# Performance work log

Hardware: AMD Instinct MI355X
Metric: run time of the kernel (lower is better)

## Reference

```python
import jax, jax.numpy as jnp
import numpy as np
from jax import lax

SEQ_LEN, N_FEAT, N_EMB, N_ENC, BATCH = 100, 18, 16, 16, 16384


def lstm(x, W_ih, W_hh, b_ih, b_hh, hidden):
    """PyTorch-convention LSTM (gates i,f,g,o), batch_first x: [B,T,I].
    Returns (h_seq [B,T,H], h_last [B,H])."""
    B = x.shape[0]
    # Precompute input projections for all timesteps: [B,T,4H]
    xg = jnp.einsum('bti,gi->btg', x, W_ih) + b_ih + b_hh
    W_hh_T = W_hh.T  # [H,4H]

    def step(carry, xg_t):
        h, c = carry
        g = xg_t + h @ W_hh_T                       # [B,4H]
        i, f, gg, o = jnp.split(g, 4, axis=-1)
        i = jax.nn.sigmoid(i)
        f = jax.nn.sigmoid(f)
        gg = jnp.tanh(gg)
        o = jax.nn.sigmoid(o)
        c = f * c + i * gg
        h = o * jnp.tanh(c)
        return (h, c), h

    h0 = jnp.zeros((B, hidden), x.dtype)
    c0 = jnp.zeros((B, hidden), x.dtype)
    (h_last, _), h_seq = lax.scan(step, (h0, c0), jnp.swapaxes(xg, 0, 1))
    return jnp.swapaxes(h_seq, 0, 1), h_last


def setup_inputs() -> dict:
    key = jax.random.key(0)
    ks = jax.random.split(key, 9)
    s1 = 1.0 / np.sqrt(N_EMB)
    s2 = 1.0 / np.sqrt(N_ENC)
    u = lambda k, shape, s: jax.random.uniform(k, shape, jnp.float32, -s, s)
    return {
        'x': jax.random.normal(ks[0], (BATCH, SEQ_LEN, N_FEAT), jnp.float32),
        'W_ih1': u(ks[1], (4 * N_EMB, N_FEAT), s1),
        'W_hh1': u(ks[2], (4 * N_EMB, N_EMB), s1),
        'b_ih1': u(ks[3], (4 * N_EMB,), s1),
        'b_hh1': u(ks[4], (4 * N_EMB,), s1),
        'W_ih2': u(ks[5], (4 * N_ENC, N_EMB), s2),
        'W_hh2': u(ks[6], (4 * N_ENC, N_ENC), s2),
        'b_ih2': u(ks[7], (4 * N_ENC,), s2),
        'b_hh2': u(ks[8], (4 * N_ENC,), s2),
    }


def reference(x, W_ih1, W_hh1, b_ih1, b_hh1, W_ih2, W_hh2, b_ih2, b_hh2):
    h1_seq, _ = lstm(x, W_ih1, W_hh1, b_ih1, b_hh1, N_EMB)
    h1_seq = jax.nn.relu(h1_seq)
    _, h2_last = lstm(h1_seq, W_ih2, W_hh2, b_ih2, b_hh2, N_ENC)
    return jax.nn.relu(h2_last)  # [B, N_ENC]
```

## Files before the change

kernel.cpp:

```cpp
#include <hip/hip_runtime.h>


typedef float f32x4 __attribute__((ext_vector_type(4)));
typedef __bf16 bf16x8 __attribute__((ext_vector_type(8)));
typedef unsigned int uint32x4 __attribute__((ext_vector_type(4)));

union FragU { bf16x8 v; unsigned short u[8]; unsigned int d[4]; uint32x4 q; };

#define MFMA16(A, B, C) __builtin_amdgcn_mfma_f32_16x16x32_bf16((A), (B), (C), 0, 0, 0)

static __device__ __forceinline__ unsigned short f2bf(float f) {
  unsigned int u = __builtin_bit_cast(unsigned int, f);
  u = u + 0x7FFFu + ((u >> 16) & 1u);
  return (unsigned short)(u >> 16);
}
static __device__ __forceinline__ float bfbits2f(unsigned short h) {
  unsigned int u = ((unsigned int)h) << 16;
  return __builtin_bit_cast(float, u);
}
static __device__ __forceinline__ float sigm(float x) {
  return __builtin_amdgcn_rcpf(1.0f + __builtin_amdgcn_exp2f(x * -1.4426950408889634f));
}
static __device__ __forceinline__ float tanh_(float x) {
  return 1.0f - 2.0f * __builtin_amdgcn_rcpf(1.0f + __builtin_amdgcn_exp2f(x * 2.8853900817779268f));
}
static __device__ __forceinline__ unsigned int split_pack(float v) {
  unsigned int u = __builtin_bit_cast(unsigned int, v);
  float hf = __builtin_bit_cast(float, u & 0xFFFF0000u);
  unsigned int l = __builtin_bit_cast(unsigned int, v - hf);
  return (u >> 16) | (l & 0xFFFF0000u);
}
static __device__ __forceinline__ void cvt_pair(float f0, float f1,
                                                unsigned int& hd, unsigned int& ld) {
  unsigned int u0 = __builtin_bit_cast(unsigned int, f0);
  unsigned int u1 = __builtin_bit_cast(unsigned int, f1);
  unsigned int h0 = u0 & 0xFFFF0000u;
  unsigned int h1 = u1 & 0xFFFF0000u;
  hd = (u0 >> 16) | h1;
  unsigned int l0 = __builtin_bit_cast(unsigned int, f0 - __builtin_bit_cast(float, h0));
  unsigned int l1 = __builtin_bit_cast(unsigned int, f1 - __builtin_bit_cast(float, h1));
  ld = (l0 >> 16) | (l1 & 0xFFFF0000u);
}

struct RawX { float2 a, b2, c, d; };

__global__ __launch_bounds__(256, 1) void enc_kernel(
    const float* __restrict__ x,
    const float* __restrict__ Wih1,
    const float* __restrict__ Whh1,
    const float* __restrict__ bih1,
    const float* __restrict__ bhh1,
    const float* __restrict__ Wih2,
    const float* __restrict__ Whh2,
    const float* __restrict__ bih2,
    const float* __restrict__ bhh2,
    float* __restrict__ out)
{
  const int lane = threadIdx.x & 63;
  const int b    = lane & 15;
  const int g    = lane >> 4;

  const int wid = (int)((blockIdx.x * blockDim.x + threadIdx.x) >> 6);
  const int b0  = wid * 16;

  FragU A1h[4], A1l[4], A2h[4], A2l[4], A3h[4], A3l[4], A4h[4], A4l[4];
  f32x4 bias1v[4], bias2v[4];
#pragma unroll
  for (int tn = 0; tn < 4; ++tn) {
    const int row = tn * 16 + b;
#pragma unroll
    for (int j = 0; j < 8; ++j) {
      const int k = 8 * g + j;
      if (k < 18) {
        const float w = Wih1[row * 18 + k];
        A1h[tn].u[j] = f2bf(w);
        A1l[tn].u[j] = f2bf(w - bfbits2f(A1h[tn].u[j]));
      } else {
        A1h[tn].u[j] = 0;
        A1l[tn].u[j] = 0;
      }
      const int kk = k >> 1;
      const float w2 = Whh1[row * 16 + kk];
      const float w3 = Wih2[row * 16 + kk];
      const float w4 = Whh2[row * 16 + kk];
      A2h[tn].u[j] = f2bf(w2); A2l[tn].u[j] = f2bf(w2 - bfbits2f(A2h[tn].u[j]));
      A3h[tn].u[j] = f2bf(w3); A3l[tn].u[j] = f2bf(w3 - bfbits2f(A3h[tn].u[j]));
      A4h[tn].u[j] = f2bf(w4); A4l[tn].u[j] = f2bf(w4 - bfbits2f(A4h[tn].u[j]));
    }
#pragma unroll
    for (int r = 0; r < 4; ++r) {
      const int u4 = tn * 16 + 4 * g + r;
      bias1v[tn][r] = bih1[u4] + bhh1[u4];
      bias2v[tn][r] = bih2[u4] + bhh2[u4];
    }
  }

  const float* const x0 = x + (size_t)(b0 + b) * 1800 + 8 * g;
  const int adv = (g == 3) ? 0 : 18;

  auto loadraw = [&](const float* p) -> RawX {
    RawX r;
    r.a = *(const float2*)p;
    if (g < 2) {
      r.b2 = *(const float2*)(p + 2);
      r.c  = *(const float2*)(p + 4);
      r.d  = *(const float2*)(p + 6);
    } else {
      r.b2 = r.c = r.d = make_float2(0.f, 0.f);
    }
    return r;
  };
  auto cvt = [&](const RawX& rw, FragU& hi, FragU& lo) {
    cvt_pair(rw.a.x, rw.a.y, hi.d[0], lo.d[0]);
    cvt_pair(rw.b2.x, rw.b2.y, hi.d[1], lo.d[1]);
    cvt_pair(rw.c.x, rw.c.y, hi.d[2], lo.d[2]);
    cvt_pair(rw.d.x, rw.d.y, hi.d[3], lo.d[3]);
  };

  RawX rw0 = loadraw(x0);
  RawX rw1 = loadraw(x0 + adv);
  RawX rw  = loadraw(x0 + 2 * adv);
  const float* xq = x0 + 3 * adv;

  FragU hb, h2b;
  hb.q  = (uint32x4){0u, 0u, 0u, 0u};
  h2b.q = (uint32x4){0u, 0u, 0u, 0u};
  float c1[4] = {0.f, 0.f, 0.f, 0.f};
  float c2[4] = {0.f, 0.f, 0.f, 0.f};
  float h2v[4] = {0.f, 0.f, 0.f, 0.f};

  FragU xch, xcl;
  cvt(rw0, xch, xcl);

  f32x4 ga[4];
#pragma unroll
  for (int tn = 0; tn < 4; ++tn) {
    f32x4 acc = MFMA16(A1h[tn].v, xch.v, bias1v[tn]);
    acc = MFMA16(A1l[tn].v, xch.v, acc);
    acc = MFMA16(A1h[tn].v, xcl.v, acc);
    acc = MFMA16(A2h[tn].v, hb.v, acc);
    acc = MFMA16(A2l[tn].v, hb.v, acc);
    ga[tn] = acc;
  }
  cvt(rw1, xch, xcl);

#pragma unroll 2
  for (int t = 0; t < 100; ++t) {
    FragU rb;
#pragma unroll
    for (int r = 0; r < 4; ++r) {
      const float iv = sigm(ga[0][r]);
      const float fv = sigm(ga[1][r]);
      const float gv = tanh_(ga[2][r]);
      const float ov = sigm(ga[3][r]);
      const float cc = fv * c1[r] + iv * gv;
      c1[r] = cc;
      const float h = ov * tanh_(cc);
      const unsigned int pk = split_pack(h);
      hb.d[r] = pk;
      rb.d[r] = (h > 0.f) ? pk : 0u;
    }

    f32x4 gb[4];
#pragma unroll
    for (int tn = 0; tn < 4; ++tn) {
      f32x4 acc = MFMA16(A4h[tn].v, h2b.v, bias2v[tn]);
      acc = MFMA16(A4l[tn].v, h2b.v, acc);
      acc = MFMA16(A3h[tn].v, rb.v, acc);
      acc = MFMA16(A3l[tn].v, rb.v, acc);
      gb[tn] = acc;
    }

    f32x4 gan[4];
#pragma unroll
    for (int tn = 0; tn < 4; ++tn) {
      f32x4 acc = MFMA16(A1h[tn].v, xch.v, bias1v[tn]);
      acc = MFMA16(A1l[tn].v, xch.v, acc);
      acc = MFMA16(A1h[tn].v, xcl.v, acc);
      acc = MFMA16(A2h[tn].v, hb.v, acc);
      acc = MFMA16(A2l[tn].v, hb.v, acc);
      gan[tn] = acc;
    }

    FragU nxh, nxl;
    cvt(rw, nxh, nxl);

    RawX rwn = loadraw((t <= 96) ? xq : x0);
    xq += adv;

#pragma unroll
    for (int r = 0; r < 4; ++r) {
      const float iv = sigm(gb[0][r]);
      const float fv = sigm(gb[1][r]);
      const float gv = tanh_(gb[2][r]);
      const float ov = sigm(gb[3][r]);
      const float cc = fv * c2[r] + iv * gv;
      c2[r] = cc;
      const float h = ov * tanh_(cc);
      h2v[r] = h;
      h2b.d[r] = split_pack(h);
    }

#pragma unroll
    for (int tn = 0; tn < 4; ++tn) ga[tn] = gan[tn];
    xch = nxh;
    xcl = nxl;
    rw = rwn;
  }

  f32x4 o;
#pragma unroll
  for (int r = 0; r < 4; ++r) o[r] = fmaxf(h2v[r], 0.f);
  *(f32x4*)(out + (size_t)(b0 + b) * 16 + 4 * g) = o;

  (void)x0;
}

extern "C" void kernel_launch(void* const* d_in, const int* in_sizes, int n_in,
                              void* d_out, int out_size, void* d_ws, size_t ws_size,
                              hipStream_t stream) {
  (void)in_sizes; (void)n_in; (void)d_ws; (void)ws_size; (void)out_size;
  enc_kernel<<<dim3(256), dim3(256), 0, stream>>>(
      (const float*)d_in[0],
      (const float*)d_in[1],
      (const float*)d_in[2],
      (const float*)d_in[3],
      (const float*)d_in[4],
      (const float*)d_in[5],
      (const float*)d_in[6],
      (const float*)d_in[7],
      (const float*)d_in[8],
      (float*)d_out);
}
```

Baseline: 270.3 us.

## Skew layer-2 LSTM activation one step behind and use v_perm for bf16 packing

Moves the layer-2 gate activation and cell update into the same per-row loop as layer 1, working on layer-2 gates computed in the previous iteration. This lets the layer-2 and layer-1 MFMA chains issue back to back while the transcendental work of both layers interleaves, which shortens the serial dependency chain per timestep. A dummy initial gate value (large negative, giving roughly zero i, f and o) seeds the pipeline, and an epilogue finishes the last layer-2 step. The bf16 hi/lo packing now uses a single byte-permute instead of shift-and-or sequences. The dummy first step gives h2 near zero rather than exactly zero, which is a small numerical risk.

Result: no change. 273.1 us (+1.0%).

```diff
diff --git a/kernel.cpp b/kernel.cpp
--- a/kernel.cpp
+++ b/kernel.cpp
@@ -28,7 +28,7 @@
   unsigned int u = __builtin_bit_cast(unsigned int, v);
   float hf = __builtin_bit_cast(float, u & 0xFFFF0000u);
   unsigned int l = __builtin_bit_cast(unsigned int, v - hf);
-  return (u >> 16) | (l & 0xFFFF0000u);
+  return __builtin_amdgcn_perm(l, u, 0x07060302u);
 }
 static __device__ __forceinline__ void cvt_pair(float f0, float f1,
                                                 unsigned int& hd, unsigned int& ld) {
@@ -36,10 +36,10 @@
   unsigned int u1 = __builtin_bit_cast(unsigned int, f1);
   unsigned int h0 = u0 & 0xFFFF0000u;
   unsigned int h1 = u1 & 0xFFFF0000u;
-  hd = (u0 >> 16) | h1;
+  hd = __builtin_amdgcn_perm(u1, u0, 0x07060302u);
   unsigned int l0 = __builtin_bit_cast(unsigned int, f0 - __builtin_bit_cast(float, h0));
   unsigned int l1 = __builtin_bit_cast(unsigned int, f1 - __builtin_bit_cast(float, h1));
-  ld = (l0 >> 16) | (l1 & 0xFFFF0000u);
+  ld = __builtin_amdgcn_perm(l1, l0, 0x07060302u);
 }
 
 struct RawX { float2 a, b2, c, d; };
@@ -110,11 +110,11 @@
     }
     return r;
   };
-  auto cvt = [&](const RawX& rw, FragU& hi, FragU& lo) {
-    cvt_pair(rw.a.x, rw.a.y, hi.d[0], lo.d[0]);
-    cvt_pair(rw.b2.x, rw.b2.y, hi.d[1], lo.d[1]);
-    cvt_pair(rw.c.x, rw.c.y, hi.d[2], lo.d[2]);
-    cvt_pair(rw.d.x, rw.d.y, hi.d[3], lo.d[3]);
+  auto cvt = [&](const RawX& rw_, FragU& hi, FragU& lo) {
+    cvt_pair(rw_.a.x, rw_.a.y, hi.d[0], lo.d[0]);
+    cvt_pair(rw_.b2.x, rw_.b2.y, hi.d[1], lo.d[1]);
+    cvt_pair(rw_.c.x, rw_.c.y, hi.d[2], lo.d[2]);
+    cvt_pair(rw_.d.x, rw_.d.y, hi.d[3], lo.d[3]);
   };
 
   RawX rw0 = loadraw(x0);
@@ -127,7 +127,6 @@
   h2b.q = (uint32x4){0u, 0u, 0u, 0u};
   float c1[4] = {0.f, 0.f, 0.f, 0.f};
   float c2[4] = {0.f, 0.f, 0.f, 0.f};
-  float h2v[4] = {0.f, 0.f, 0.f, 0.f};
 
   FragU xch, xcl;
   cvt(rw0, xch, xcl);
@@ -143,6 +142,12 @@
     ga[tn] = acc;
   }
   cvt(rw1, xch, xcl);
+
+  f32x4 gb[4];
+  gb[0] = (f32x4){-1e3f, -1e3f, -1e3f, -1e3f};
+  gb[1] = gb[0];
+  gb[2] = (f32x4){0.f, 0.f, 0.f, 0.f};
+  gb[3] = gb[0];
 
 #pragma unroll 2
   for (int t = 0; t < 100; ++t) {
@@ -159,16 +164,24 @@
       const unsigned int pk = split_pack(h);
       hb.d[r] = pk;
       rb.d[r] = (h > 0.f) ? pk : 0u;
-    }
-
-    f32x4 gb[4];
+      const float iv2 = sigm(gb[0][r]);
+      const float fv2 = sigm(gb[1][r]);
+      const float gv2 = tanh_(gb[2][r]);
+      const float ov2 = sigm(gb[3][r]);
+      const float dd = fv2 * c2[r] + iv2 * gv2;
+      c2[r] = dd;
+      const float h2 = ov2 * tanh_(dd);
+      h2b.d[r] = split_pack(h2);
+    }
+
+    f32x4 gbn[4];
 #pragma unroll
     for (int tn = 0; tn < 4; ++tn) {
       f32x4 acc = MFMA16(A4h[tn].v, h2b.v, bias2v[tn]);
       acc = MFMA16(A4l[tn].v, h2b.v, acc);
       acc = MFMA16(A3h[tn].v, rb.v, acc);
       acc = MFMA16(A3l[tn].v, rb.v, acc);
-      gb[tn] = acc;
+      gbn[tn] = acc;
     }
 
     f32x4 gan[4];
@@ -189,20 +202,7 @@
     xq += adv;
 
 #pragma unroll
-    for (int r = 0; r < 4; ++r) {
-      const float iv = sigm(gb[0][r]);
-      const float fv = sigm(gb[1][r]);
-      const float gv = tanh_(gb[2][r]);
-      const float ov = sigm(gb[3][r]);
-      const float cc = fv * c2[r] + iv * gv;
-      c2[r] = cc;
-      const float h = ov * tanh_(cc);
-      h2v[r] = h;
-      h2b.d[r] = split_pack(h);
-    }
-
-#pragma unroll
-    for (int tn = 0; tn < 4; ++tn) ga[tn] = gan[tn];
+    for (int tn = 0; tn < 4; ++tn) { ga[tn] = gan[tn]; gb[tn] = gbn[tn]; }
     xch = nxh;
     xcl = nxl;
     rw = rwn;
@@ -210,7 +210,15 @@
 
   f32x4 o;
 #pragma unroll
-  for (int r = 0; r < 4; ++r) o[r] = fmaxf(h2v[r], 0.f);
+  for (int r = 0; r < 4; ++r) {
+    const float iv2 = sigm(gb[0][r]);
+    const float fv2 = sigm(gb[1][r]);
+    const float gv2 = tanh_(gb[2][r]);
+    const float ov2 = sigm(gb[3][r]);
+    const float dd = fv2 * c2[r] + iv2 * gv2;
+    const float h2 = ov2 * tanh_(dd);
+    o[r] = fmaxf(h2, 0.f);
+  }
   *(f32x4*)(out + (size_t)(b0 + b) * 16 + 4 * g) = o;
 
   (void)x0;
```
